# Performance work log

Hardware: AMD Instinct MI355X
Metric: run time of the kernel (lower is better)

The kernel has to match this reference:

```python
import jax, jax.numpy as jnp
import numpy as np

BN_EPS = 1e-5
NUM_ROUTING_ITERS = 3


def _bn(x, gamma, beta, axes):
    # training-mode batch norm (torch default train mode): batch statistics
    mean = x.mean(axes, keepdims=True)
    var = x.var(axes, keepdims=True)
    return (x - mean) * jax.lax.rsqrt(var + BN_EPS) * gamma + beta


def _squash(x):
    # squash over last dim: sn * x / ((1+sn) * sqrt(sn))
    sn = jnp.sum(x * x, axis=-1, keepdims=True)
    return sn * x / ((1.0 + sn) * jnp.sqrt(sn))


def setup_inputs() -> dict:
    key = jax.random.key(0)
    ks = jax.random.split(key, 16)
    B, N = 4, 2048          # batch, num_points
    P, Q = 1024, 16         # prim_caps_size, prim_vec_size
    L, V = 64, 64           # latent_caps_size, latent_vec_size
    OUT = 40
    s = 0.02
    return {
        "x": jax.random.normal(ks[0], (B, 3, N), dtype=jnp.float32),
        # ConvLayer
        "w1": jax.random.normal(ks[1], (64, 3), dtype=jnp.float32) * s,
        "b1": jnp.zeros((64,), jnp.float32),
        "g1": jnp.ones((64,), jnp.float32),
        "be1": jnp.zeros((64,), jnp.float32),
        "w2": jax.random.normal(ks[2], (128, 64), dtype=jnp.float32) * s,
        "b2": jnp.zeros((128,), jnp.float32),
        "g2": jnp.ones((128,), jnp.float32),
        "be2": jnp.zeros((128,), jnp.float32),
        # PrimaryPointCapsLayer: Q parallel conv1d(128->P, k=1)+BN branches, stacked
        "w3": jax.random.normal(ks[3], (Q, P, 128), dtype=jnp.float32) * s,
        "b3": jnp.zeros((Q, P), jnp.float32),
        "g3": jnp.ones((Q, P), jnp.float32),
        "be3": jnp.zeros((Q, P), jnp.float32),
        # LatentCapsLayer routing weights
        "Wr": jax.random.normal(ks[4], (L, P, V, Q), dtype=jnp.float32) * 0.01,
        # classifier head
        "fc_w": jax.random.normal(ks[5], (OUT, L * V), dtype=jnp.float32) * s,
        "fc_b": jnp.zeros((OUT,), jnp.float32),
    }


def reference(x, w1, b1, g1, be1, w2, b2, g2, be2, w3, b3, g3, be3, Wr, fc_w, fc_b):
    B = x.shape[0]
    # ConvLayer: two 1x1 conv1d + BN + ReLU
    h = jnp.einsum("oc,bcn->bon", w1, x) + b1[None, :, None]
    h = jax.nn.relu(_bn(h, g1[None, :, None], be1[None, :, None], (0, 2)))
    h = jnp.einsum("oc,bcn->bon", w2, h) + b2[None, :, None]
    h = jax.nn.relu(_bn(h, g2[None, :, None], be2[None, :, None], (0, 2)))  # [B,128,N]

    # PrimaryPointCapsLayer: Q branches of conv1d+BN+global maxpool, vectorized
    u = jnp.einsum("qpc,bcn->bqpn", w3, h) + b3[None, :, :, None]  # [B,Q,P,N]
    u = _bn(u, g3[None, :, :, None], be3[None, :, :, None], (0, 3))
    u = u.max(axis=-1)                      # global maxpool -> [B,Q,P]
    u = jnp.transpose(u, (0, 2, 1))         # stack dim=2 in torch -> [B,P,Q]
    u = _squash(u)                          # squash over prim_vec

    # LatentCapsLayer dynamic routing
    u_hat = jnp.einsum("lpvq,bpq->blpv", Wr, u)   # [B,L,P,V]
    u_hat_d = jax.lax.stop_gradient(u_hat)
    L, P = Wr.shape[0], Wr.shape[1]
    b_ij = jnp.zeros((B, L, P), u_hat.dtype)
    for _ in range(NUM_ROUTING_ITERS - 1):
        c_ij = jax.nn.softmax(b_ij, axis=1)
        v_j = _squash(jnp.einsum("blp,blpv->blv", c_ij, u_hat_d))
        b_ij = b_ij + jnp.einsum("blv,blpv->blp", v_j, u_hat_d)
    c_ij = jax.nn.softmax(b_ij, axis=1)
    v_j = _squash(jnp.einsum("blp,blpv->blv", c_ij, u_hat))  # [B,L,V]

    presence = jnp.linalg.norm(v_j, axis=2)                   # [B,L]
    logits = v_j.reshape(B, -1) @ fc_w.T + fc_b               # [B,OUT]
    return (logits, presence)
```

## Files before the change

kernel.cpp:

```cpp
#include <hip/hip_runtime.h>
#include <math.h>

#define BN_EPS 1e-5f

typedef __attribute__((ext_vector_type(8))) _Float16 half8;
typedef __attribute__((ext_vector_type(4))) _Float16 half4;
typedef __attribute__((ext_vector_type(4))) float f32x4;
#define SPLIT_S  2048.0f
#define INV_S    (1.0f/2048.0f)


__global__ __launch_bounds__(256) void k_pre(const float* __restrict__ x,
        const float* __restrict__ w1, float* __restrict__ y1,
        float* __restrict__ mean, float* __restrict__ inv,
        const float* __restrict__ w3, const float* __restrict__ g3,
        _Float16* __restrict__ hi, _Float16* __restrict__ lo) {
    const int t = threadIdx.x;
    if (blockIdx.x < 512) {
        int base = blockIdx.x * 256 + t;
#pragma unroll
        for (int it = 0; it < 4; ++it) {
            int i = (base + it * 131072) * 4;
            float4 d = *reinterpret_cast<const float4*>(w3 + i);
            float sgn = (g3[i >> 7] < 0.f) ? -1.f : 1.f;
            float vs[4] = {d.x * sgn, d.y * sgn, d.z * sgn, d.w * sgn};
            half4 h4, l4;
#pragma unroll
            for (int j = 0; j < 4; ++j) {
                _Float16 h = (_Float16)vs[j];
                h4[j] = h;
                l4[j] = (_Float16)((vs[j] - (float)h) * SPLIT_S);
            }
            *reinterpret_cast<half4*>(hi + i) = h4;
            *reinterpret_cast<half4*>(lo + i) = l4;
        }
        return;
    }
    const int o = blockIdx.x - 512;
    const float wa = w1[o*3+0], wb = w1[o*3+1], wc = w1[o*3+2];
    float s = 0.f, ss = 0.f;
#pragma unroll
    for (int it = 0; it < 8; ++it) {
        int i = it * 256 + t;
        int b = i >> 9, n4 = (i & 511) * 4;
        const float* xb = x + (size_t)b * 6144 + n4;
        float4 x0 = *(const float4*)(xb);
        float4 x1 = *(const float4*)(xb + 2048);
        float4 x2 = *(const float4*)(xb + 4096);
        float4 r;
        r.x = wa*x0.x + wb*x1.x + wc*x2.x;
        r.y = wa*x0.y + wb*x1.y + wc*x2.y;
        r.z = wa*x0.z + wb*x1.z + wc*x2.z;
        r.w = wa*x0.w + wb*x1.w + wc*x2.w;
        *(float4*)(y1 + o * 8192 + i * 4) = r;
        s += r.x + r.y + r.z + r.w;
        ss = fmaf(r.x, r.x, fmaf(r.y, r.y, fmaf(r.z, r.z, fmaf(r.w, r.w, ss))));
    }
    __shared__ float rs[256], rss[256];
    rs[t] = s; rss[t] = ss;
    __syncthreads();
    for (int off = 128; off > 0; off >>= 1) {
        if (t < off) { rs[t] += rs[t+off]; rss[t] += rss[t+off]; }
        __syncthreads();
    }
    if (t == 0) {
        float m = rs[0] * (1.f/8192.f);
        float var = rss[0] * (1.f/8192.f) - m*m;
        mean[o] = m;
        inv[o]  = rsqrtf(var + BN_EPS);
    }
}

__global__ void k_stats(const float* __restrict__ y, float* __restrict__ mean,
                        float* __restrict__ inv) {
    int c = blockIdx.x, t = threadIdx.x;
    float s = 0.f, ss = 0.f;
    const float4* src = (const float4*)(y + c * 8192);
    for (int i = t; i < 2048; i += 256) {
        float4 v = src[i];
        s += v.x + v.y + v.z + v.w;
        ss = fmaf(v.x, v.x, fmaf(v.y, v.y, fmaf(v.z, v.z, fmaf(v.w, v.w, ss))));
    }
    __shared__ float rs[256], rss[256];
    rs[t] = s; rss[t] = ss;
    __syncthreads();
    for (int off = 128; off > 0; off >>= 1) {
        if (t < off) { rs[t] += rs[t+off]; rss[t] += rss[t+off]; }
        __syncthreads();
    }
    if (t == 0) {
        float m = rs[0] * (1.f/8192.f);
        float var = rss[0] * (1.f/8192.f) - m*m;
        mean[c] = m;
        inv[c]  = rsqrtf(var + BN_EPS);
    }
}

__global__ __launch_bounds__(256) void k_conv2(const float* __restrict__ y1,
        const float* __restrict__ w2,
        const float* __restrict__ mean1, const float* __restrict__ inv1,
        const float* __restrict__ g1, const float* __restrict__ be1,
        float* __restrict__ y2) {
    __shared__ float sc1[64], sh1[64];
    const int t = threadIdx.x;
    if (t < 64) {
        float sc = inv1[t] * g1[t];
        sc1[t] = sc;
        sh1[t] = be1[t] - mean1[t] * sc;
    }
    __syncthreads();
    int bn0 = (blockIdx.x * 256 + t) * 4;
    int og0 = blockIdx.y * 4;
    float4 acc[4];
#pragma unroll
    for (int j = 0; j < 4; ++j) acc[j] = float4{0.f,0.f,0.f,0.f};
    for (int c = 0; c < 64; ++c) {
        float4 hv = *(const float4*)(y1 + c*8192 + bn0);
        float sc = sc1[c], sh = sh1[c];
        hv.x = fmaxf(fmaf(hv.x, sc, sh), 0.f);
        hv.y = fmaxf(fmaf(hv.y, sc, sh), 0.f);
        hv.z = fmaxf(fmaf(hv.z, sc, sh), 0.f);
        hv.w = fmaxf(fmaf(hv.w, sc, sh), 0.f);
#pragma unroll
        for (int j = 0; j < 4; ++j) {
            float w = w2[(og0+j)*64 + c];
            acc[j].x = fmaf(w, hv.x, acc[j].x); acc[j].y = fmaf(w, hv.y, acc[j].y);
            acc[j].z = fmaf(w, hv.z, acc[j].z); acc[j].w = fmaf(w, hv.w, acc[j].w);
        }
    }
#pragma unroll
    for (int j = 0; j < 4; ++j) *(float4*)(y2 + (og0+j)*8192 + bn0) = acc[j];
}

__global__ __launch_bounds__(256) void k_h2t_split(const float* __restrict__ y2,
        const float* __restrict__ mean, const float* __restrict__ inv,
        const float* __restrict__ g, const float* __restrict__ be,
        _Float16* __restrict__ hi, _Float16* __restrict__ lo) {
    __shared__ float tile[64][65];
    const int t = threadIdx.x;
    const int bn0 = blockIdx.x * 64, c0 = blockIdx.y * 64;
#pragma unroll
    for (int r = 0; r < 4; ++r) {
        int idx = r * 256 + t;
        int cl = idx >> 4, bn4 = (idx & 15) * 4;
        int c = c0 + cl;
        float sc = inv[c] * g[c];
        float sh = be[c] - mean[c] * sc;
        float4 d = *(const float4*)(y2 + (size_t)c * 8192 + bn0 + bn4);
        tile[cl][bn4  ] = fmaxf(fmaf(d.x, sc, sh), 0.f);
        tile[cl][bn4+1] = fmaxf(fmaf(d.y, sc, sh), 0.f);
        tile[cl][bn4+2] = fmaxf(fmaf(d.z, sc, sh), 0.f);
        tile[cl][bn4+3] = fmaxf(fmaf(d.w, sc, sh), 0.f);
    }
    __syncthreads();
#pragma unroll
    for (int r = 0; r < 4; ++r) {
        int idx = r * 256 + t;
        int bnl = idx >> 4, c4 = (idx & 15) * 4;
        half4 h4, l4;
#pragma unroll
        for (int j = 0; j < 4; ++j) {
            float v = tile[c4 + j][bnl];
            _Float16 h = (_Float16)v;
            h4[j] = h;
            l4[j] = (_Float16)((v - (float)h) * SPLIT_S);
        }
        size_t o = (size_t)(bn0 + bnl) * 128 + c0 + c4;
        *reinterpret_cast<half4*>(hi + o) = h4;
        *reinterpret_cast<half4*>(lo + o) = l4;
    }
}

__global__ __launch_bounds__(256, 2) void k_caps(
        const _Float16* __restrict__ w3h, const _Float16* __restrict__ w3l,
        const _Float16* __restrict__ h2h, const _Float16* __restrict__ h2l,
        float* __restrict__ umax,
        float* __restrict__ usum_b, float* __restrict__ usumsq_b) {
    const int lane = threadIdx.x & 63, wave = threadIdx.x >> 6;
    const int b = blockIdx.y;
    const int mrow = blockIdx.x * 128 + wave * 32;
    const int r16 = lane & 15, kq = lane >> 4;

    __shared__ _Float16 Bs[2][2][8][64][8];

    half8 Ah[2][4], Al[2][4];
#pragma unroll
    for (int mt = 0; mt < 2; ++mt) {
        const size_t base = (size_t)(mrow + mt*16 + r16) * 128 + kq * 8;
#pragma unroll
        for (int ks = 0; ks < 4; ++ks) {
            Ah[mt][ks] = *reinterpret_cast<const half8*>(w3h + base + ks*32);
            Al[mt][ks] = *reinterpret_cast<const half8*>(w3l + base + ks*32);
        }
    }
    float mx[2][4], sm[2][4], sq[2][4];
#pragma unroll
    for (int mt = 0; mt < 2; ++mt)
#pragma unroll
        for (int r = 0; r < 4; ++r) {
            mx[mt][r] = -3.4e38f; sm[mt][r] = 0.f; sq[mt][r] = 0.f;
        }

    const int u0 = wave * 2;
    const size_t srow = (size_t)(b*2048 + r16) * 128 + wave * 32 + kq * 8;

    {
#pragma unroll
        for (int g = 0; g < 2; ++g) {
            const size_t a = srow + (size_t)g * 16 * 128;
            *reinterpret_cast<half8*>(&Bs[0][g][u0  ][lane][0]) = *reinterpret_cast<const half8*>(h2h + a);
            *reinterpret_cast<half8*>(&Bs[0][g][u0+1][lane][0]) = *reinterpret_cast<const half8*>(h2l + a);
        }
    }
    __syncthreads();

    for (int nt = 0; nt < 64; ++nt) {
        const int buf = nt & 1;
        const int ntn = (nt + 1 < 64) ? nt + 1 : nt;
        const size_t snext = srow + (size_t)ntn * 32 * 128;
        half8 g0h = *reinterpret_cast<const half8*>(h2h + snext);
        half8 g0l = *reinterpret_cast<const half8*>(h2l + snext);
        half8 g1h = *reinterpret_cast<const half8*>(h2h + snext + 2048);
        half8 g1l = *reinterpret_cast<const half8*>(h2l + snext + 2048);

#pragma unroll
        for (int g = 0; g < 2; ++g) {
            f32x4 acc[2], accx[2];
#pragma unroll
            for (int mt = 0; mt < 2; ++mt) { acc[mt] = f32x4{0.f,0.f,0.f,0.f}; accx[mt] = f32x4{0.f,0.f,0.f,0.f}; }
#pragma unroll
            for (int ks = 0; ks < 4; ++ks) {
                half8 Bh = *reinterpret_cast<const half8*>(&Bs[buf][g][ks*2  ][lane][0]);
                half8 Bl = *reinterpret_cast<const half8*>(&Bs[buf][g][ks*2+1][lane][0]);
#pragma unroll
                for (int mt = 0; mt < 2; ++mt) {
                    acc[mt]  = __builtin_amdgcn_mfma_f32_16x16x32_f16(Ah[mt][ks], Bh, acc[mt], 0, 0, 0);
                    accx[mt] = __builtin_amdgcn_mfma_f32_16x16x32_f16(Ah[mt][ks], Bl, accx[mt], 0, 0, 0);
                    accx[mt] = __builtin_amdgcn_mfma_f32_16x16x32_f16(Al[mt][ks], Bh, accx[mt], 0, 0, 0);
                }
            }
#pragma unroll
            for (int mt = 0; mt < 2; ++mt)
#pragma unroll
                for (int r = 0; r < 4; ++r) {
                    float v = fmaf(accx[mt][r], INV_S, acc[mt][r]);
                    mx[mt][r] = fmaxf(mx[mt][r], v);
                    sm[mt][r] += v;
                    sq[mt][r] = fmaf(v, v, sq[mt][r]);
                }
        }
        *reinterpret_cast<half8*>(&Bs[buf^1][0][u0  ][lane][0]) = g0h;
        *reinterpret_cast<half8*>(&Bs[buf^1][0][u0+1][lane][0]) = g0l;
        *reinterpret_cast<half8*>(&Bs[buf^1][1][u0  ][lane][0]) = g1h;
        *reinterpret_cast<half8*>(&Bs[buf^1][1][u0+1][lane][0]) = g1l;
        __syncthreads();
    }

#pragma unroll
    for (int off = 8; off >= 1; off >>= 1)
#pragma unroll
        for (int mt = 0; mt < 2; ++mt)
#pragma unroll
            for (int r = 0; r < 4; ++r) {
                mx[mt][r] = fmaxf(mx[mt][r], __shfl_xor(mx[mt][r], off));
                sm[mt][r] += __shfl_xor(sm[mt][r], off);
                sq[mt][r] += __shfl_xor(sq[mt][r], off);
            }
    if (r16 == 0) {
#pragma unroll
        for (int mt = 0; mt < 2; ++mt)
#pragma unroll
            for (int r = 0; r < 4; ++r) {
                int qp = mrow + mt*16 + kq*4 + r;
                umax[b*16384 + qp]     = mx[mt][r];
                usum_b[b*16384 + qp]   = sm[mt][r];
                usumsq_b[b*16384 + qp] = sq[mt][r];
            }
    }
}

__global__ __launch_bounds__(256) void k_uhat(const float* __restrict__ Wr,
                                              const float* __restrict__ umax,
                                              const float* __restrict__ usum_b,
                                              const float* __restrict__ usumsq_b,
                                              const float* __restrict__ g3,
                                              const float* __restrict__ be3,
                                              float* __restrict__ uhat2,
                                              float* __restrict__ s1p) {
    const int t = threadIdx.x;
    const int pblk = blockIdx.x, l = blockIdx.y;
    __shared__ float wr[4][64][20];
    __shared__ float us_all[32][4][16];
    const int bb = t >> 6, v = t & 63;

    if (t < 128) {
        int p = t & 31, b2 = t >> 5;
        int pg = pblk * 32 + p;
        float ub[16]; float sn = 0.f;
#pragma unroll
        for (int q = 0; q < 16; ++q) {
            int qp = q * 1024 + pg;
            float s  = usum_b[qp] + usum_b[16384+qp] + usum_b[32768+qp] + usum_b[49152+qp];
            float ss = usumsq_b[qp] + usumsq_b[16384+qp] + usumsq_b[32768+qp] + usumsq_b[49152+qp];
            float g  = g3[qp];
            float sgn = (g < 0.f) ? -1.f : 1.f;
            float mean  = sgn * s * (1.f/8192.f);
            float var   = ss * (1.f/8192.f) - mean*mean;
            float scale = g * rsqrtf(var + BN_EPS);
            float val = sgn * umax[b2*16384 + qp];
            float vb = (val - mean) * scale + be3[qp];
            ub[q] = vb; sn = fmaf(vb, vb, sn);
        }
        float f = sqrtf(sn) / (1.f + sn);
#pragma unroll
        for (int q = 0; q < 16; ++q) us_all[p][b2][q] = ub[q] * f;
    }

    float s1acc = 0.f;
    for (int sub = 0; sub < 8; ++sub) {
        const int p0 = pblk * 32 + sub * 4;
        const float* src = Wr + ((size_t)l * 1024 + p0) * 1024;
        if (sub) __syncthreads();
#pragma unroll
        for (int it = 0; it < 4; ++it) {
            float4 d = *(const float4*)(src + (it*256 + t) * 4);
            int vv = t >> 2, q0 = (t & 3) * 4;
            *(float4*)&wr[it][vv][q0] = d;
        }
        __syncthreads();
#pragma unroll
        for (int p = 0; p < 4; ++p) {
            float acc = 0.f;
            const int pl = sub * 4 + p;
#pragma unroll
            for (int q4 = 0; q4 < 4; ++q4) {
                float4 wf = *(const float4*)&wr[p][v][q4*4];
                float4 uf = *(const float4*)&us_all[pl][bb][q4*4];
                acc = fmaf(wf.x, uf.x, acc);
                acc = fmaf(wf.y, uf.y, acc);
                acc = fmaf(wf.z, uf.z, acc);
                acc = fmaf(wf.w, uf.w, acc);
            }
            uhat2[(((size_t)bb * 1024 + p0 + p) * 64 + l) * 64 + v] = acc;
            s1acc += acc;
        }
    }
    s1p[(((size_t)pblk * 4 + bb) * 64 + l) * 64 + v] = s1acc;
}

__global__ void k_s1red(const float* __restrict__ s1p, float* __restrict__ vout) {
    const int wv = blockIdx.x;
    const int b = wv >> 6, l = wv & 63;
    const int v = threadIdx.x;
    float acc = 0.f;
#pragma unroll
    for (int pblk = 0; pblk < 32; ++pblk)
        acc += s1p[(((size_t)pblk * 4 + b) * 64 + l) * 64 + v];
    float s = acc * (1.f/64.f);
    float sn = s * s;
#pragma unroll
    for (int off = 32; off >= 1; off >>= 1) sn += __shfl_xor(sn, off);
    vout[wv * 64 + v] = s * sqrtf(sn) / (1.f + sn);
}

__global__ __launch_bounds__(256) void k_route(const float* __restrict__ uhat2,
                                               const float* __restrict__ vin,
                                               float* __restrict__ bij,
                                               float* __restrict__ part, const int read_b) {
    const int blk = blockIdx.x;
    const int b = blk >> 7, ch = blk & 127;
    const int p0 = ch * 8;
    const int t = threadIdx.x;
    const int v = t & 63, w = t >> 6;
    __shared__ float uh[64][68];
    __shared__ float vs[64][68];
    __shared__ float bl[64];
    {
        const float* src = vin + b * 4096;
        for (int i = t; i < 1024; i += 256) {
            float4 d = *(const float4*)(src + i * 4);
            int l = i >> 4, v0 = (i & 15) * 4;
            vs[l][v0] = d.x; vs[l][v0+1] = d.y; vs[l][v0+2] = d.z; vs[l][v0+3] = d.w;
        }
    }
    float sacc[16];
#pragma unroll
    for (int j = 0; j < 16; ++j) sacc[j] = 0.f;

    for (int pp = 0; pp < 8; ++pp) {
        const int p = p0 + pp;
        __syncthreads();
        const float* src = uhat2 + ((size_t)b * 1024 + p) * 4096;
        for (int i = t; i < 1024; i += 256) {
            float4 d = *(const float4*)(src + i * 4);
            int l = i >> 4, v0 = (i & 15) * 4;
            uh[l][v0] = d.x; uh[l][v0+1] = d.y; uh[l][v0+2] = d.z; uh[l][v0+3] = d.w;
        }
        __syncthreads();
#pragma unroll
        for (int i = 0; i < 16; ++i) {
            const int l = w * 16 + i;
            float prod = uh[l][v] * vs[l][v];
#pragma unroll
            for (int off = 32; off >= 1; off >>= 1) prod += __shfl_xor(prod, off);
            if (v == 0) {
                float bb = prod;
                if (read_b) bb += bij[(b * 64 + l) * 1024 + p];
                bl[l] = bb;
                if (!read_b) bij[(b * 64 + l) * 1024 + p] = bb;
            }
        }
        __syncthreads();
        float xv = bl[v];
        float m = xv;
#pragma unroll
        for (int off = 32; off >= 1; off >>= 1) m = fmaxf(m, __shfl_xor(m, off));
        float e = expf(xv - m);
        float sgm = e;
#pragma unroll
        for (int off = 32; off >= 1; off >>= 1) sgm += __shfl_xor(sgm, off);
        float c = e / sgm;
#pragma unroll
        for (int j = 0; j < 16; ++j) {
            const int l = j * 4 + w;
            float cl = __shfl(c, l);
            sacc[j] = fmaf(cl, uh[l][v], sacc[j]);
        }
    }
#pragma unroll
    for (int j = 0; j < 16; ++j) {
        const int l = j * 4 + w;
        part[((size_t)(b * 128 + ch) * 64 + l) * 64 + v] = sacc[j];
    }
}

__global__ void k_red_squash(const float* __restrict__ part, float* __restrict__ vout,
                             float* __restrict__ pres) {
    const int wv = blockIdx.x;
    const int b = wv >> 6, l = wv & 63;
    const int v = threadIdx.x;
    float acc = 0.f;
    for (int ch = 0; ch < 128; ++ch) acc += part[((size_t)(b * 128 + ch) * 64 + l) * 64 + v];
    float sn = acc * acc;
#pragma unroll
    for (int off = 32; off >= 1; off >>= 1) sn += __shfl_xor(sn, off);
    vout[wv * 64 + v] = acc * sqrtf(sn) / (1.f + sn);
    if (pres != nullptr && v == 0) pres[wv] = sn / (1.f + sn);
}

__global__ void k_logits(const float* __restrict__ vj, const float* __restrict__ fcw,
                         const float* __restrict__ fcb, float* __restrict__ out) {
    int wv = blockIdx.x * 4 + (threadIdx.x >> 6);
    int lane = threadIdx.x & 63;
    int b = wv / 40, o = wv % 40;
    const float* xv = vj + b * 4096;
    const float* wr = fcw + (size_t)o * 4096;
    float acc = 0.f;
    for (int i = lane; i < 4096; i += 64) acc = fmaf(xv[i], wr[i], acc);
#pragma unroll
    for (int off = 32; off >= 1; off >>= 1) acc += __shfl_xor(acc, off);
    if (lane == 0) out[b * 40 + o] = acc + fcb[o];
}

extern "C" void kernel_launch(void* const* d_in, const int* in_sizes, int n_in,
                              void* d_out, int out_size, void* d_ws, size_t ws_size,
                              hipStream_t stream) {
    const float* x   = (const float*)d_in[0];
    const float* w1  = (const float*)d_in[1];
    const float* g1  = (const float*)d_in[3];
    const float* be1 = (const float*)d_in[4];
    const float* w2  = (const float*)d_in[5];
    const float* g2  = (const float*)d_in[7];
    const float* be2 = (const float*)d_in[8];
    const float* w3  = (const float*)d_in[9];
    const float* g3  = (const float*)d_in[11];
    const float* be3 = (const float*)d_in[12];
    const float* Wr  = (const float*)d_in[13];
    const float* fcw = (const float*)d_in[14];
    const float* fcb = (const float*)d_in[15];
    float* out = (float*)d_out;

    float* ws       = (float*)d_ws;
    float* y1       = ws;
    float* y2       = y1 + 524288;
    float* mean1    = y2 + 1048576;
    float* inv1     = mean1 + 64;
    float* mean2    = inv1 + 64;
    float* inv2     = mean2 + 128;
    float* umax     = inv2 + 128;
    float* usum_b   = umax + 65536;
    float* usumsq_b = usum_b + 65536;
    float* u_unused = usumsq_b + 65536;
    float* v1       = u_unused + 65536;
    float* v2       = v1 + 16384;
    float* vj       = v2 + 16384;
    float* bij      = vj + 16384;
    float* s1p      = bij + 262144;
    float* part     = s1p + 524288;
    float* uhat2    = part + 2097152;
    _Float16* w3h = (_Float16*)uhat2;
    _Float16* w3l = w3h + 2097152;
    _Float16* h2h = w3l + 2097152;
    _Float16* h2l = h2h + 1048576;

    k_pre<<<576, 256, 0, stream>>>(x, w1, y1, mean1, inv1, w3, g3, w3h, w3l);
    k_conv2<<<dim3(8, 32), 256, 0, stream>>>(y1, w2, mean1, inv1, g1, be1, y2);
    k_stats<<<128, 256, 0, stream>>>(y2, mean2, inv2);
    k_h2t_split<<<dim3(128, 2), 256, 0, stream>>>(y2, mean2, inv2, g2, be2, h2h, h2l);
    k_caps<<<dim3(128, 4), 256, 0, stream>>>(w3h, w3l, h2h, h2l, umax, usum_b, usumsq_b);
    k_uhat<<<dim3(32, 64), 256, 0, stream>>>(Wr, umax, usum_b, usumsq_b, g3, be3, uhat2, s1p);
    k_s1red<<<256, 64, 0, stream>>>(s1p, v1);
    k_route<<<512, 256, 0, stream>>>(uhat2, v1, bij, part, 0);
    k_red_squash<<<256, 64, 0, stream>>>(part, v2, nullptr);
    k_route<<<512, 256, 0, stream>>>(uhat2, v2, bij, part, 1);
    k_red_squash<<<256, 64, 0, stream>>>(part, vj, out + 160);
    k_logits<<<40, 256, 0, stream>>>(vj, fcw, fcb, out);
}
```

Before: 686.3 us.

## Use direct global-to-LDS loads in conv GEMM and drop Wr LDS staging

Measured after the change: 693.7 us. No clear change (+1.1%).

```diff
diff --git a/kernel.cpp b/kernel.cpp
--- a/kernel.cpp
+++ b/kernel.cpp
@@ -9,6 +9,10 @@
 #define SPLIT_S  2048.0f
 #define INV_S    (1.0f/2048.0f)
 
+
+#define GLDS(gp, lp) __builtin_amdgcn_global_load_lds( \
+        (const __attribute__((address_space(1))) void*)(gp), \
+        (__attribute__((address_space(3))) void*)(lp), 16, 0, 0)
 
 __global__ __launch_bounds__(256) void k_pre(const float* __restrict__ x,
         const float* __restrict__ w1, float* __restrict__ y1,
@@ -205,23 +209,22 @@
     const size_t srow = (size_t)(b*2048 + r16) * 128 + wave * 32 + kq * 8;
 
     {
-#pragma unroll
-        for (int g = 0; g < 2; ++g) {
-            const size_t a = srow + (size_t)g * 16 * 128;
-            *reinterpret_cast<half8*>(&Bs[0][g][u0  ][lane][0]) = *reinterpret_cast<const half8*>(h2h + a);
-            *reinterpret_cast<half8*>(&Bs[0][g][u0+1][lane][0]) = *reinterpret_cast<const half8*>(h2l + a);
-        }
+        GLDS(h2h + srow,        &Bs[0][0][u0  ][0][0]);
+        GLDS(h2l + srow,        &Bs[0][0][u0+1][0][0]);
+        GLDS(h2h + srow + 2048, &Bs[0][1][u0  ][0][0]);
+        GLDS(h2l + srow + 2048, &Bs[0][1][u0+1][0][0]);
     }
     __syncthreads();
 
     for (int nt = 0; nt < 64; ++nt) {
         const int buf = nt & 1;
-        const int ntn = (nt + 1 < 64) ? nt + 1 : nt;
-        const size_t snext = srow + (size_t)ntn * 32 * 128;
-        half8 g0h = *reinterpret_cast<const half8*>(h2h + snext);
-        half8 g0l = *reinterpret_cast<const half8*>(h2l + snext);
-        half8 g1h = *reinterpret_cast<const half8*>(h2h + snext + 2048);
-        half8 g1l = *reinterpret_cast<const half8*>(h2l + snext + 2048);
+        if (nt + 1 < 64) {
+            const size_t snext = srow + (size_t)(nt + 1) * 32 * 128;
+            GLDS(h2h + snext,        &Bs[buf^1][0][u0  ][0][0]);
+            GLDS(h2l + snext,        &Bs[buf^1][0][u0+1][0][0]);
+            GLDS(h2h + snext + 2048, &Bs[buf^1][1][u0  ][0][0]);
+            GLDS(h2l + snext + 2048, &Bs[buf^1][1][u0+1][0][0]);
+        }
 
 #pragma unroll
         for (int g = 0; g < 2; ++g) {
@@ -249,10 +252,6 @@
                     sq[mt][r] = fmaf(v, v, sq[mt][r]);
                 }
         }
-        *reinterpret_cast<half8*>(&Bs[buf^1][0][u0  ][lane][0]) = g0h;
-        *reinterpret_cast<half8*>(&Bs[buf^1][0][u0+1][lane][0]) = g0l;
-        *reinterpret_cast<half8*>(&Bs[buf^1][1][u0  ][lane][0]) = g1h;
-        *reinterpret_cast<half8*>(&Bs[buf^1][1][u0+1][lane][0]) = g1l;
         __syncthreads();
     }
 
@@ -289,7 +288,6 @@
                                               float* __restrict__ s1p) {
     const int t = threadIdx.x;
     const int pblk = blockIdx.x, l = blockIdx.y;
-    __shared__ float wr[4][64][20];
     __shared__ float us_all[32][4][16];
     const int bb = t >> 6, v = t & 63;
 
@@ -315,35 +313,32 @@
 #pragma unroll
         for (int q = 0; q < 16; ++q) us_all[p][b2][q] = ub[q] * f;
     }
+    __syncthreads();
 
     float s1acc = 0.f;
-    for (int sub = 0; sub < 8; ++sub) {
-        const int p0 = pblk * 32 + sub * 4;
-        const float* src = Wr + ((size_t)l * 1024 + p0) * 1024;
-        if (sub) __syncthreads();
-#pragma unroll
-        for (int it = 0; it < 4; ++it) {
-            float4 d = *(const float4*)(src + (it*256 + t) * 4);
-            int vv = t >> 2, q0 = (t & 3) * 4;
-            *(float4*)&wr[it][vv][q0] = d;
-        }
-        __syncthreads();
-#pragma unroll
-        for (int p = 0; p < 4; ++p) {
-            float acc = 0.f;
-            const int pl = sub * 4 + p;
-#pragma unroll
-            for (int q4 = 0; q4 < 4; ++q4) {
-                float4 wf = *(const float4*)&wr[p][v][q4*4];
-                float4 uf = *(const float4*)&us_all[pl][bb][q4*4];
-                acc = fmaf(wf.x, uf.x, acc);
-                acc = fmaf(wf.y, uf.y, acc);
-                acc = fmaf(wf.z, uf.z, acc);
-                acc = fmaf(wf.w, uf.w, acc);
-            }
-            uhat2[(((size_t)bb * 1024 + p0 + p) * 64 + l) * 64 + v] = acc;
-            s1acc += acc;
-        }
+    const float* wbase = Wr + ((size_t)l * 1024 + pblk * 32) * 1024 + v * 16;
+#pragma unroll 4
+    for (int pl = 0; pl < 32; ++pl) {
+        const float* src = wbase + (size_t)pl * 1024;
+        float4 w0 = *(const float4*)(src);
+        float4 w1 = *(const float4*)(src + 4);
+        float4 w2 = *(const float4*)(src + 8);
+        float4 w3 = *(const float4*)(src + 12);
+        float4 u0 = *(const float4*)&us_all[pl][bb][0];
+        float4 u1 = *(const float4*)&us_all[pl][bb][4];
+        float4 u2 = *(const float4*)&us_all[pl][bb][8];
+        float4 u3 = *(const float4*)&us_all[pl][bb][12];
+        float acc = 0.f;
+        acc = fmaf(w0.x, u0.x, acc); acc = fmaf(w0.y, u0.y, acc);
+        acc = fmaf(w0.z, u0.z, acc); acc = fmaf(w0.w, u0.w, acc);
+        acc = fmaf(w1.x, u1.x, acc); acc = fmaf(w1.y, u1.y, acc);
+        acc = fmaf(w1.z, u1.z, acc); acc = fmaf(w1.w, u1.w, acc);
+        acc = fmaf(w2.x, u2.x, acc); acc = fmaf(w2.y, u2.y, acc);
+        acc = fmaf(w2.z, u2.z, acc); acc = fmaf(w2.w, u2.w, acc);
+        acc = fmaf(w3.x, u3.x, acc); acc = fmaf(w3.y, u3.y, acc);
+        acc = fmaf(w3.z, u3.z, acc); acc = fmaf(w3.w, u3.w, acc);
+        uhat2[(((size_t)bb * 1024 + pblk * 32 + pl) * 64 + l) * 64 + v] = acc;
+        s1acc += acc;
     }
     s1p[(((size_t)pblk * 4 + bb) * 64 + l) * 64 + v] = s1acc;
 }
```
